# Optimization experiments

Measured on AMD Instinct MI355X. Metric: run time of the kernel, lower is better.

Reference implementation:

```python
import jax, jax.numpy as jnp
import numpy as np

BATCH, SEQ, H_IN, N_STATE, H_OUT = 16, 4096, 128, 256, 128
RMIN, RMAX, MAX_PHASE = 0.9, 1.0, 6.283


def setup_inputs() -> dict:
    key = jax.random.key(0)
    ks = jax.random.split(key, 9)
    u = jax.random.normal(ks[0], (BATCH, SEQ, H_IN), jnp.float32)
    # LRU exponential parameterization init (matches torch __init__)
    u1 = jax.random.uniform(ks[1], (N_STATE,), jnp.float32)
    u2 = jax.random.uniform(ks[2], (N_STATE,), jnp.float32)
    nu_log = jnp.log(-0.5 * jnp.log(u1 * (RMAX + RMIN) * (RMAX - RMIN) + RMIN ** 2))
    theta_log = jnp.log(MAX_PHASE * u2)
    lam_abs = jnp.exp(-jnp.exp(nu_log))
    gamma_log = jnp.log(jnp.sqrt(1.0 - lam_abs ** 2))
    s2in = np.sqrt(2.0 * H_IN).astype(np.float32)
    B_re = jax.random.normal(ks[3], (N_STATE, H_IN), jnp.float32) / s2in
    B_im = jax.random.normal(ks[4], (N_STATE, H_IN), jnp.float32) / s2in
    sst = np.sqrt(float(N_STATE)).astype(np.float32)
    C_re = jax.random.normal(ks[5], (H_OUT, N_STATE), jnp.float32) / sst
    C_im = jax.random.normal(ks[6], (H_OUT, N_STATE), jnp.float32) / sst
    D = jax.random.normal(ks[7], (H_OUT, H_IN), jnp.float32) / np.sqrt(float(H_IN)).astype(np.float32)
    return dict(u=u, nu_log=nu_log, theta_log=theta_log, gamma_log=gamma_log,
                B_re=B_re, B_im=B_im, C_re=C_re, C_im=C_im, D=D)


def _combine(a, b):
    # complex affine composition: (l, x) o (l', x') -> (l*l', l'*x + x')
    l1r, l1i, x1r, x1i = a
    l2r, l2i, x2r, x2i = b
    lr = l1r * l2r - l1i * l2i
    li = l1r * l2i + l1i * l2r
    xr = l2r * x1r - l2i * x1i + x2r
    xi = l2r * x1i + l2i * x1r + x2i
    return (lr, li, xr, xi)


def reference(u, nu_log, theta_log, gamma_log, B_re, B_im, C_re, C_im, D):
    lam_mod = jnp.exp(-jnp.exp(nu_log))          # |lambda|, [N]
    th = jnp.exp(theta_log)
    lam_re = lam_mod * jnp.cos(th)
    lam_im = lam_mod * jnp.sin(th)
    gammas = jnp.exp(gamma_log)                  # [N]
    # input projection Bu_t = gamma * (B @ u_t), complex -> real/imag parts
    Bu_re = jnp.einsum('blh,nh->bln', u, B_re) * gammas  # [B,L,N]
    Bu_im = jnp.einsum('blh,nh->bln', u, B_im) * gammas
    Bsz, L, N = Bu_re.shape
    lr = jnp.broadcast_to(lam_re, (Bsz, L, N))
    li = jnp.broadcast_to(lam_im, (Bsz, L, N))
    # parallel scan of x_t = lambda * x_{t-1} + Bu_t, x0 = 0
    _, _, xr, xi = jax.lax.associative_scan(_combine, (lr, li, Bu_re, Bu_im), axis=1)
    zero = jnp.zeros((Bsz, 1, N), u.dtype)
    pre_re = jnp.concatenate([zero, xr[:, :-1]], axis=1)  # states[:, :-1]
    pre_im = jnp.concatenate([zero, xi[:, :-1]], axis=1)
    # y_t = Re(C x_{t-1}) + D u_t
    y = (jnp.einsum('bln,on->blo', pre_re, C_re)
         - jnp.einsum('bln,on->blo', pre_im, C_im)
         + jnp.einsum('blh,oh->blo', u, D))
    return y
```

## Files before the change

kernel.cpp:

```cpp
#include <hip/hip_runtime.h>
#include <math.h>

#define BATCH 16
#define SEQ   4096
#define HIN   128
#define NST   256
#define HOUT  128
#define CL    32
#define NC    (SEQ/CL)
#define ROWS  (BATCH*SEQ)
#define KTOT  640
#define NPRE  512

typedef __attribute__((ext_vector_type(8))) short short8;
typedef __attribute__((ext_vector_type(4))) float f32x4;

__device__ inline unsigned short f2bf(float f) {
  union { float f; unsigned u; } v; v.f = f;
  unsigned r = v.u + 0x7FFFu + ((v.u >> 16) & 1u);
  return (unsigned short)(r >> 16);
}
__device__ inline float bf2f(unsigned short s) {
  union { unsigned u; float f; } v; v.u = ((unsigned)s) << 16;
  return v.f;
}
__device__ inline float bits2f(unsigned u) {
  union { unsigned u; float f; } v; v.u = u; return v.f;
}

__global__ __launch_bounds__(256) void k_prep(
    const float* __restrict__ nu_log, const float* __restrict__ theta_log,
    const float* __restrict__ gamma_log,
    const float* __restrict__ Bre, const float* __restrict__ Bim,
    const float* __restrict__ Cre, const float* __restrict__ Cim,
    const float* __restrict__ Dm,
    float* __restrict__ lamre, float* __restrict__ lamim,
    unsigned* __restrict__ lamPk,
    unsigned short* __restrict__ Wb, unsigned short* __restrict__ W) {
  int idx = blockIdx.x*256 + threadIdx.x;
  if (idx < NST) {
    float lm = expf(-expf(nu_log[idx]));
    float th = expf(theta_log[idx]);
    float lr = lm * cosf(th), li = lm * sinf(th);
    lamre[idx] = lr; lamim[idx] = li;
    float pr = 1.f, pi = 0.f;
    for (int j = 0; j < CL; ++j) {
      lamPk[j*NST + idx] = ((unsigned)f2bf(pi) << 16) | (unsigned)f2bf(pr);
      float nr = pr*lr - pi*li;
      float ni = pr*li + pi*lr;
      pr = nr; pi = ni;
    }
  }
  if (idx < 512*HIN) {
    int r = idx >> 7, h = idx & 127;
    int g = r >> 7;
    int w = r & 127;
    int n = g*64 + (w & 63);
    float gm = expf(gamma_log[n]);
    float v = (w < 64) ? Bre[n*HIN + h] : Bim[n*HIN + h];
    Wb[idx] = f2bf(gm * v);
  }
  if (idx < HOUT*KTOT) {
    int o = idx / KTOT, k = idx - o*KTOT;
    float v;
    if (k < NST)        v =  Cre[o*NST + k];
    else if (k < 2*NST) v = -Cim[o*NST + (k - NST)];
    else                v =  Dm[o*HIN + (k - 2*NST)];
    W[idx] = f2bf(v);
  }
}

union SharedBu {
  unsigned short B[128][136];
  unsigned short stgb[2][32][136];
};
__global__ __launch_bounds__(256) void k_bu(
    const float* __restrict__ u, const unsigned short* __restrict__ Wb,
    const float* __restrict__ lamre, const float* __restrict__ lamim,
    unsigned short* __restrict__ preL,
    float* __restrict__ S_re, float* __restrict__ S_im) {
  __shared__ unsigned short Asl[128][136];
  __shared__ SharedBu sh;
  int tid = threadIdx.x;
  int row0 = blockIdx.x * 128;
  int wid = tid >> 6, lane = tid & 63;
  int lm = lane & 15, lq = lane >> 4;
  int m0 = (wid >> 1) * 64, n0 = (wid & 1) * 64;
  int b = row0 >> 12;
  int cbase = (row0 & 4095) >> 5;
#pragma unroll
  for (int cc = 0; cc < 8; ++cc) {
    int ch = cc*256 + tid;
    int r = ch >> 4, h0 = (ch & 15) * 8;
    const float* src = u + (size_t)(row0 + r)*HIN + h0;
    float4 v0 = *(const float4*)src;
    float4 v1 = *(const float4*)(src + 4);
    unsigned short o[8];
    o[0]=f2bf(v0.x); o[1]=f2bf(v0.y); o[2]=f2bf(v0.z); o[3]=f2bf(v0.w);
    o[4]=f2bf(v1.x); o[5]=f2bf(v1.y); o[6]=f2bf(v1.z); o[7]=f2bf(v1.w);
    *(short8*)&Asl[r][h0] = *(const short8*)o;
  }
  for (int g = 0; g < 4; ++g) {
    __syncthreads();
#pragma unroll
    for (int cc = 0; cc < 8; ++cc) {
      int ch = cc*256 + tid;
      int r = ch >> 4, h0 = (ch & 15) * 8;
      *(short8*)&sh.B[r][h0] = *(const short8*)&Wb[(size_t)(g*128 + r)*HIN + h0];
    }
    __syncthreads();
    f32x4 acc[4][4];
#pragma unroll
    for (int i = 0; i < 4; ++i)
#pragma unroll
      for (int j = 0; j < 4; ++j) acc[i][j] = (f32x4)0.f;
#pragma unroll
    for (int ks = 0; ks < 4; ++ks) {
      int k0 = ks*32 + lq*8;
      short8 a[4], bb[4];
#pragma unroll
      for (int i = 0; i < 4; ++i) a[i] = *(const short8*)&Asl[m0 + i*16 + lm][k0];
#pragma unroll
      for (int j = 0; j < 4; ++j) bb[j] = *(const short8*)&sh.B[n0 + j*16 + lm][k0];
#pragma unroll
      for (int i = 0; i < 4; ++i)
#pragma unroll
        for (int j = 0; j < 4; ++j)
          acc[i][j] = __builtin_amdgcn_mfma_f32_16x16x32_bf16(a[i], bb[j], acc[i][j], 0, 0, 0);
    }
    for (int p = 0; p < 2; ++p) {
      __syncthreads();
#pragma unroll
      for (int ii = 0; ii < 2; ++ii) {
        int i = 2*p + ii;
#pragma unroll
        for (int j = 0; j < 4; ++j)
#pragma unroll
          for (int r = 0; r < 4; ++r) {
            int trow = ii*16 + lq*4 + r;
            sh.stgb[wid >> 1][trow][n0 + j*16 + lm] = f2bf(acc[i][j][r]);
          }
      }
      __syncthreads();
      if (tid < 128) {
        int buf = tid >> 6, nl = tid & 63;
        int ng = g*64 + nl;
        float lr = lamre[ng], li = lamim[ng];
        float rr[CL], ri[CL];
#pragma unroll
        for (int t = 0; t < CL; ++t) {
          rr[t] = bf2f(sh.stgb[buf][t][nl]);
          ri[t] = bf2f(sh.stgb[buf][t][64 + nl]);
        }
        float sr = 0.f, si = 0.f;
#pragma unroll
        for (int t = 0; t < CL; ++t) {
          sh.stgb[buf][t][nl]      = f2bf(sr);
          sh.stgb[buf][t][64 + nl] = f2bf(si);
          float nr = lr*sr - li*si + rr[t];
          float ni = lr*si + li*sr + ri[t];
          sr = nr; si = ni;
        }
        int c = cbase + buf*2 + p;
        int idx = (b*NC + c)*NST + ng;
        S_re[idx] = sr; S_im[idx] = si;
      }
      __syncthreads();
#pragma unroll
      for (int q = 0; q < 4; ++q) {
        int uidx = q*256 + tid;
        int buf = uidx >> 9;
        int rem = uidx & 511;
        int t   = rem >> 4;
        int seg = rem & 15;
        int im  = seg >> 3;
        int c0  = (seg & 7)*8 + im*64;
        int row = row0 + buf*64 + p*32 + t;
        int dcol = im*256 + g*64 + (seg & 7)*8;
        *(short8*)&preL[(size_t)row*NPRE + dcol] = *(const short8*)&sh.stgb[buf][t][c0];
      }
    }
  }
}

__global__ __launch_bounds__(64) void k_scan(
    const float* __restrict__ S_re, const float* __restrict__ S_im,
    const float* __restrict__ lamre, const float* __restrict__ lamim,
    unsigned* __restrict__ X0Pk) {
  int b = blockIdx.x >> 2;
  int n = (blockIdx.x & 3) * 64 + threadIdx.x;
  float ar = lamre[n], ai = lamim[n];
#pragma unroll
  for (int s = 0; s < 5; ++s) { float nr = ar*ar - ai*ai, ni = 2.f*ar*ai; ar = nr; ai = ni; }
  const float* Sr = S_re + (size_t)b*NC*NST + n;
  const float* Si = S_im + (size_t)b*NC*NST + n;
  unsigned* Xp = X0Pk + (size_t)b*NC*NST + n;
  float Are[16], Aim[16], Bre[16], Bim[16];
#pragma unroll
  for (int cc = 0; cc < 16; ++cc) { Are[cc] = Sr[cc*NST]; Aim[cc] = Si[cc*NST]; }
  float xr = 0.f, xi = 0.f;
#pragma unroll
  for (int seg = 0; seg < 8; ++seg) {
    if (seg < 7) {
      const float* pr = Sr + (size_t)(seg+1)*16*NST;
      const float* pi = Si + (size_t)(seg+1)*16*NST;
      if (seg & 1) {
#pragma unroll
        for (int cc = 0; cc < 16; ++cc) { Are[cc] = pr[cc*NST]; Aim[cc] = pi[cc*NST]; }
      } else {
#pragma unroll
        for (int cc = 0; cc < 16; ++cc) { Bre[cc] = pr[cc*NST]; Bim[cc] = pi[cc*NST]; }
      }
    }
#pragma unroll
    for (int cc = 0; cc < 16; ++cc) {
      Xp[(size_t)(seg*16 + cc)*NST] = ((unsigned)f2bf(xi) << 16) | (unsigned)f2bf(xr);
      float cr = (seg & 1) ? Bre[cc] : Are[cc];
      float ci = (seg & 1) ? Bim[cc] : Aim[cc];
      float nr = ar*xr - ai*xi + cr;
      float ni = ar*xi + ai*xr + ci;
      xr = nr; xi = ni;
    }
  }
}

__global__ __launch_bounds__(256) void k_out2(
    const unsigned short* __restrict__ preL, const float* __restrict__ u,
    const unsigned short* __restrict__ W,
    const unsigned* __restrict__ lamPk, const unsigned* __restrict__ X0Pk,
    float* __restrict__ y) {
  __shared__ unsigned short Asl[128][136];
  __shared__ unsigned short Bsl[128][136];
  int tid = threadIdx.x;
  int row0 = blockIdx.x * 128;
  int wid = tid >> 6, lane = tid & 63;
  int lm = lane & 15, lq = lane >> 4;
  int m0 = wid * 32;
  f32x4 acc[2][8];
#pragma unroll
  for (int i = 0; i < 2; ++i)
#pragma unroll
    for (int j = 0; j < 8; ++j) acc[i][j] = (f32x4)0.f;
  for (int s = 0; s < 5; ++s) {
    __syncthreads();
#pragma unroll
    for (int cc = 0; cc < 8; ++cc) {
      int ch = cc*256 + tid;
      int r = ch >> 4, h0 = (ch & 15) * 8;
      *(short8*)&Bsl[r][h0] = *(const short8*)&W[(size_t)r*KTOT + s*128 + h0];
    }
    if (s < 4) {
#pragma unroll
      for (int cc = 0; cc < 8; ++cc) {
        int ch = cc*256 + tid;
        int r = ch >> 4, h0 = (ch & 15) * 8;
        int grow = row0 + r;
        int j32 = r & 31;
        int cidx = grow >> 5;
        int n = ((s & 1) << 7) + h0;
        short8 loc = *(const short8*)&preL[(size_t)grow*NPRE + s*128 + h0];
        uint4 lp0 = *(const uint4*)&lamPk[j32*NST + n];
        uint4 lp1 = *(const uint4*)&lamPk[j32*NST + n + 4];
        uint4 xp0 = *(const uint4*)&X0Pk[(size_t)cidx*NST + n];
        uint4 xp1 = *(const uint4*)&X0Pk[(size_t)cidx*NST + n + 4];
        unsigned lps[8] = {lp0.x, lp0.y, lp0.z, lp0.w, lp1.x, lp1.y, lp1.z, lp1.w};
        unsigned xps[8] = {xp0.x, xp0.y, xp0.z, xp0.w, xp1.x, xp1.y, xp1.z, xp1.w};
        unsigned short o[8];
#pragma unroll
        for (int e = 0; e < 8; ++e) {
          float lr = bits2f(lps[e] << 16);
          float li = bits2f(lps[e] & 0xFFFF0000u);
          float xr = bits2f(xps[e] << 16);
          float xi = bits2f(xps[e] & 0xFFFF0000u);
          float lv = bf2f((unsigned short)loc[e]);
          float v = (s < 2) ? (lv + lr*xr - li*xi)
                            : (lv + lr*xi + li*xr);
          o[e] = f2bf(v);
        }
        *(short8*)&Asl[r][h0] = *(const short8*)o;
      }
    } else {
#pragma unroll
      for (int cc = 0; cc < 8; ++cc) {
        int ch = cc*256 + tid;
        int r = ch >> 4, h0 = (ch & 15) * 8;
        const float* src = u + (size_t)(row0 + r)*HIN + h0;
        float4 v0 = *(const float4*)src;
        float4 v1 = *(const float4*)(src + 4);
        unsigned short o[8];
        o[0]=f2bf(v0.x); o[1]=f2bf(v0.y); o[2]=f2bf(v0.z); o[3]=f2bf(v0.w);
        o[4]=f2bf(v1.x); o[5]=f2bf(v1.y); o[6]=f2bf(v1.z); o[7]=f2bf(v1.w);
        *(short8*)&Asl[r][h0] = *(const short8*)o;
      }
    }
    __syncthreads();
#pragma unroll
    for (int ks = 0; ks < 4; ++ks) {
      int k0 = ks*32 + lq*8;
      short8 a[2], bb[8];
#pragma unroll
      for (int i = 0; i < 2; ++i) a[i] = *(const short8*)&Asl[m0 + i*16 + lm][k0];
#pragma unroll
      for (int j = 0; j < 8; ++j) bb[j] = *(const short8*)&Bsl[j*16 + lm][k0];
#pragma unroll
      for (int i = 0; i < 2; ++i)
#pragma unroll
        for (int j = 0; j < 8; ++j)
          acc[i][j] = __builtin_amdgcn_mfma_f32_16x16x32_bf16(a[i], bb[j], acc[i][j], 0, 0, 0);
    }
  }
#pragma unroll
  for (int i = 0; i < 2; ++i)
#pragma unroll
    for (int j = 0; j < 8; ++j)
#pragma unroll
      for (int r = 0; r < 4; ++r)
        y[(size_t)(row0 + m0 + i*16 + lq*4 + r)*HOUT + j*16 + lm] = acc[i][j][r];
}

extern "C" void kernel_launch(void* const* d_in, const int* in_sizes, int n_in,
                              void* d_out, int out_size, void* d_ws, size_t ws_size,
                              hipStream_t stream) {
  const float* u         = (const float*)d_in[0];
  const float* nu_log    = (const float*)d_in[1];
  const float* theta_log = (const float*)d_in[2];
  const float* gamma_log = (const float*)d_in[3];
  const float* B_re      = (const float*)d_in[4];
  const float* B_im      = (const float*)d_in[5];
  const float* C_re      = (const float*)d_in[6];
  const float* C_im      = (const float*)d_in[7];
  const float* Dm        = (const float*)d_in[8];
  float* y = (float*)d_out;
  char* ws = (char*)d_ws;

  size_t off = 0;
  float* lamre = (float*)(ws + off);            off += 1024;
  float* lamim = (float*)(ws + off);            off += 1024;
  unsigned* lamPk = (unsigned*)(ws + off);      off += 32768;
  unsigned short* Wb = (unsigned short*)(ws + off); off += 131072;
  unsigned short* W  = (unsigned short*)(ws + off); off += 163840;
  unsigned short* preL = (unsigned short*)(ws + off); off += (size_t)ROWS*NPRE*2;
  float* S_re = (float*)(ws + off);             off += 2097152;
  float* S_im = (float*)(ws + off);             off += 2097152;
  unsigned* X0Pk = (unsigned*)(ws + off);       off += 2097152;

  k_prep<<<320, 256, 0, stream>>>(nu_log, theta_log, gamma_log, B_re, B_im,
                                  C_re, C_im, Dm, lamre, lamim, lamPk, Wb, W);
  k_bu<<<ROWS/128, 256, 0, stream>>>(u, Wb, lamre, lamim, preL, S_re, S_im);
  k_scan<<<64, 64, 0, stream>>>(S_re, S_im, lamre, lamim, X0Pk);
  k_out2<<<ROWS/128, 256, 0, stream>>>(preL, u, W, lamPk, X0Pk, y);
}
```

Before: 162.4 us.

## Recompute Bu projection in output kernel instead of materializing local states

The first pass now computes only the per-chunk end states and no longer writes the large bf16 local-state buffer (preL, 64 MB). The output kernel recomputes the B projection per 64-row tile, runs the intra-chunk recurrence seeded with the carried-in state, stages the states in shared memory, and feeds them straight into the C GEMM. Tile sizes are halved to 64 rows with launch-bounds occupancy hints. This removes a large global write and read at the cost of doing the input GEMM twice and running a serial scan inside the output kernel.

Result: slower. 174.9 us (+7.7%).

```diff
diff --git a/kernel.cpp b/kernel.cpp
--- a/kernel.cpp
+++ b/kernel.cpp
@@ -10,7 +10,6 @@
 #define NC    (SEQ/CL)
 #define ROWS  (BATCH*SEQ)
 #define KTOT  640
-#define NPRE  512
 
 typedef __attribute__((ext_vector_type(8))) short short8;
 typedef __attribute__((ext_vector_type(4))) float f32x4;
@@ -35,21 +34,13 @@
     const float* __restrict__ Cre, const float* __restrict__ Cim,
     const float* __restrict__ Dm,
     float* __restrict__ lamre, float* __restrict__ lamim,
-    unsigned* __restrict__ lamPk,
-    unsigned short* __restrict__ Wb, unsigned short* __restrict__ W) {
+    unsigned short* __restrict__ Wb, unsigned short* __restrict__ W2) {
   int idx = blockIdx.x*256 + threadIdx.x;
   if (idx < NST) {
     float lm = expf(-expf(nu_log[idx]));
     float th = expf(theta_log[idx]);
-    float lr = lm * cosf(th), li = lm * sinf(th);
-    lamre[idx] = lr; lamim[idx] = li;
-    float pr = 1.f, pi = 0.f;
-    for (int j = 0; j < CL; ++j) {
-      lamPk[j*NST + idx] = ((unsigned)f2bf(pi) << 16) | (unsigned)f2bf(pr);
-      float nr = pr*lr - pi*li;
-      float ni = pr*li + pi*lr;
-      pr = nr; pi = ni;
-    }
+    lamre[idx] = lm * cosf(th);
+    lamim[idx] = lm * sinf(th);
   }
   if (idx < 512*HIN) {
     int r = idx >> 7, h = idx & 127;
@@ -63,33 +54,36 @@
   if (idx < HOUT*KTOT) {
     int o = idx / KTOT, k = idx - o*KTOT;
     float v;
-    if (k < NST)        v =  Cre[o*NST + k];
-    else if (k < 2*NST) v = -Cim[o*NST + (k - NST)];
-    else                v =  Dm[o*HIN + (k - 2*NST)];
-    W[idx] = f2bf(v);
-  }
-}
-
-union SharedBu {
-  unsigned short B[128][136];
+    if (k < 512) {
+      int g = k >> 7, kk = k & 127;
+      int n = g*64 + (kk & 63);
+      v = (kk < 64) ? Cre[o*NST + n] : -Cim[o*NST + n];
+    } else {
+      v = Dm[o*HIN + (k - 512)];
+    }
+    W2[idx] = f2bf(v);
+  }
+}
+
+union SharedK1 {
+  unsigned short B[128][72];
   unsigned short stgb[2][32][136];
 };
-__global__ __launch_bounds__(256) void k_bu(
+__global__ __launch_bounds__(256, 4) void k_bu(
     const float* __restrict__ u, const unsigned short* __restrict__ Wb,
     const float* __restrict__ lamre, const float* __restrict__ lamim,
-    unsigned short* __restrict__ preL,
     float* __restrict__ S_re, float* __restrict__ S_im) {
-  __shared__ unsigned short Asl[128][136];
-  __shared__ SharedBu sh;
+  __shared__ unsigned short Asl[64][136];
+  __shared__ SharedK1 sh;
   int tid = threadIdx.x;
-  int row0 = blockIdx.x * 128;
+  int row0 = blockIdx.x * 64;
   int wid = tid >> 6, lane = tid & 63;
   int lm = lane & 15, lq = lane >> 4;
-  int m0 = (wid >> 1) * 64, n0 = (wid & 1) * 64;
+  int m0 = wid * 16;
   int b = row0 >> 12;
   int cbase = (row0 & 4095) >> 5;
 #pragma unroll
-  for (int cc = 0; cc < 8; ++cc) {
+  for (int cc = 0; cc < 4; ++cc) {
     int ch = cc*256 + tid;
     int r = ch >> 4, h0 = (ch & 15) * 8;
     const float* src = u + (size_t)(row0 + r)*HIN + h0;
@@ -101,84 +95,58 @@
     *(short8*)&Asl[r][h0] = *(const short8*)o;
   }
   for (int g = 0; g < 4; ++g) {
-    __syncthreads();
-#pragma unroll
-    for (int cc = 0; cc < 8; ++cc) {
-      int ch = cc*256 + tid;
-      int r = ch >> 4, h0 = (ch & 15) * 8;
-      *(short8*)&sh.B[r][h0] = *(const short8*)&Wb[(size_t)(g*128 + r)*HIN + h0];
-    }
-    __syncthreads();
-    f32x4 acc[4][4];
-#pragma unroll
-    for (int i = 0; i < 4; ++i)
-#pragma unroll
-      for (int j = 0; j < 4; ++j) acc[i][j] = (f32x4)0.f;
-#pragma unroll
-    for (int ks = 0; ks < 4; ++ks) {
-      int k0 = ks*32 + lq*8;
-      short8 a[4], bb[4];
-#pragma unroll
-      for (int i = 0; i < 4; ++i) a[i] = *(const short8*)&Asl[m0 + i*16 + lm][k0];
-#pragma unroll
-      for (int j = 0; j < 4; ++j) bb[j] = *(const short8*)&sh.B[n0 + j*16 + lm][k0];
-#pragma unroll
-      for (int i = 0; i < 4; ++i)
-#pragma unroll
-        for (int j = 0; j < 4; ++j)
-          acc[i][j] = __builtin_amdgcn_mfma_f32_16x16x32_bf16(a[i], bb[j], acc[i][j], 0, 0, 0);
-    }
-    for (int p = 0; p < 2; ++p) {
-      __syncthreads();
-#pragma unroll
-      for (int ii = 0; ii < 2; ++ii) {
-        int i = 2*p + ii;
-#pragma unroll
-        for (int j = 0; j < 4; ++j)
-#pragma unroll
-          for (int r = 0; r < 4; ++r) {
-            int trow = ii*16 + lq*4 + r;
-            sh.stgb[wid >> 1][trow][n0 + j*16 + lm] = f2bf(acc[i][j][r]);
-          }
-      }
-      __syncthreads();
-      if (tid < 128) {
-        int buf = tid >> 6, nl = tid & 63;
-        int ng = g*64 + nl;
-        float lr = lamre[ng], li = lamim[ng];
-        float rr[CL], ri[CL];
-#pragma unroll
-        for (int t = 0; t < CL; ++t) {
-          rr[t] = bf2f(sh.stgb[buf][t][nl]);
-          ri[t] = bf2f(sh.stgb[buf][t][64 + nl]);
+    f32x4 accB[8];
+#pragma unroll
+    for (int j = 0; j < 8; ++j) accB[j] = (f32x4)0.f;
+    for (int kh = 0; kh < 2; ++kh) {
+      __syncthreads();
+#pragma unroll
+      for (int cc = 0; cc < 4; ++cc) {
+        int ch = cc*256 + tid;
+        int r = ch >> 3, h0 = (ch & 7) * 8;
+        *(short8*)&sh.B[r][h0] = *(const short8*)&Wb[(size_t)(g*128 + r)*HIN + kh*64 + h0];
+      }
+      __syncthreads();
+#pragma unroll
+      for (int ks2 = 0; ks2 < 2; ++ks2) {
+        int k0 = (kh*2 + ks2)*32 + lq*8;
+        short8 a = *(const short8*)&Asl[m0 + lm][k0];
+#pragma unroll
+        for (int j = 0; j < 8; ++j) {
+          short8 bb = *(const short8*)&sh.B[j*16 + lm][k0 - kh*64];
+          accB[j] = __builtin_amdgcn_mfma_f32_16x16x32_bf16(a, bb, accB[j], 0, 0, 0);
         }
-        float sr = 0.f, si = 0.f;
-#pragma unroll
-        for (int t = 0; t < CL; ++t) {
-          sh.stgb[buf][t][nl]      = f2bf(sr);
-          sh.stgb[buf][t][64 + nl] = f2bf(si);
-          float nr = lr*sr - li*si + rr[t];
-          float ni = lr*si + li*sr + ri[t];
-          sr = nr; si = ni;
-        }
-        int c = cbase + buf*2 + p;
-        int idx = (b*NC + c)*NST + ng;
-        S_re[idx] = sr; S_im[idx] = si;
-      }
-      __syncthreads();
-#pragma unroll
-      for (int q = 0; q < 4; ++q) {
-        int uidx = q*256 + tid;
-        int buf = uidx >> 9;
-        int rem = uidx & 511;
-        int t   = rem >> 4;
-        int seg = rem & 15;
-        int im  = seg >> 3;
-        int c0  = (seg & 7)*8 + im*64;
-        int row = row0 + buf*64 + p*32 + t;
-        int dcol = im*256 + g*64 + (seg & 7)*8;
-        *(short8*)&preL[(size_t)row*NPRE + dcol] = *(const short8*)&sh.stgb[buf][t][c0];
-      }
+      }
+    }
+    __syncthreads();
+#pragma unroll
+    for (int j = 0; j < 8; ++j)
+#pragma unroll
+      for (int r = 0; r < 4; ++r) {
+        int row = m0 + lq*4 + r;
+        sh.stgb[row >> 5][row & 31][j*16 + lm] = f2bf(accB[j][r]);
+      }
+    __syncthreads();
+    if (tid < 128) {
+      int buf = tid >> 6, nl = tid & 63;
+      int ng = g*64 + nl;
+      float lr = lamre[ng], li = lamim[ng];
+      float rr[CL], ri[CL];
+#pragma unroll
+      for (int t = 0; t < CL; ++t) {
+        rr[t] = bf2f(sh.stgb[buf][t][nl]);
+        ri[t] = bf2f(sh.stgb[buf][t][64 + nl]);
+      }
+      float sr = 0.f, si = 0.f;
+#pragma unroll
+      for (int t = 0; t < CL; ++t) {
+        float nr = lr*sr - li*si + rr[t];
+        float ni = lr*si + li*sr + ri[t];
+        sr = nr; si = ni;
+      }
+      int c = cbase + buf;
+      int idx = (b*NC + c)*NST + ng;
+      S_re[idx] = sr; S_im[idx] = si;
     }
   }
 }
@@ -224,98 +192,137 @@
   }
 }
 
-__global__ __launch_bounds__(256) void k_out2(
-    const unsigned short* __restrict__ preL, const float* __restrict__ u,
-    const unsigned short* __restrict__ W,
-    const unsigned* __restrict__ lamPk, const unsigned* __restrict__ X0Pk,
+__global__ __launch_bounds__(256, 2) void k_out3(
+    const float* __restrict__ u, const unsigned short* __restrict__ Wb,
+    const unsigned short* __restrict__ W2,
+    const float* __restrict__ lamre, const float* __restrict__ lamim,
+    const unsigned* __restrict__ X0Pk,
     float* __restrict__ y) {
-  __shared__ unsigned short Asl[128][136];
-  __shared__ unsigned short Bsl[128][136];
+  __shared__ unsigned short Asl[64][136];
+  __shared__ unsigned short Bh[128][72];
+  __shared__ unsigned short stgb[2][32][136];
+  __shared__ unsigned short preS[64][136];
   int tid = threadIdx.x;
-  int row0 = blockIdx.x * 128;
+  int row0 = blockIdx.x * 64;
   int wid = tid >> 6, lane = tid & 63;
   int lm = lane & 15, lq = lane >> 4;
-  int m0 = wid * 32;
-  f32x4 acc[2][8];
-#pragma unroll
-  for (int i = 0; i < 2; ++i)
-#pragma unroll
-    for (int j = 0; j < 8; ++j) acc[i][j] = (f32x4)0.f;
-  for (int s = 0; s < 5; ++s) {
-    __syncthreads();
-#pragma unroll
-    for (int cc = 0; cc < 8; ++cc) {
+  int m0 = wid * 16;
+  int c0 = row0 >> 5;
+#pragma unroll
+  for (int cc = 0; cc < 4; ++cc) {
+    int ch = cc*256 + tid;
+    int r = ch >> 4, h0 = (ch & 15) * 8;
+    const float* src = u + (size_t)(row0 + r)*HIN + h0;
+    float4 v0 = *(const float4*)src;
+    float4 v1 = *(const float4*)(src + 4);
+    unsigned short o[8];
+    o[0]=f2bf(v0.x); o[1]=f2bf(v0.y); o[2]=f2bf(v0.z); o[3]=f2bf(v0.w);
+    o[4]=f2bf(v1.x); o[5]=f2bf(v1.y); o[6]=f2bf(v1.z); o[7]=f2bf(v1.w);
+    *(short8*)&Asl[r][h0] = *(const short8*)o;
+  }
+  f32x4 accY[8];
+#pragma unroll
+  for (int j = 0; j < 8; ++j) accY[j] = (f32x4)0.f;
+  for (int g = 0; g < 4; ++g) {
+    f32x4 accB[8];
+#pragma unroll
+    for (int j = 0; j < 8; ++j) accB[j] = (f32x4)0.f;
+    for (int kh = 0; kh < 2; ++kh) {
+      __syncthreads();
+#pragma unroll
+      for (int cc = 0; cc < 4; ++cc) {
+        int ch = cc*256 + tid;
+        int r = ch >> 3, h0 = (ch & 7) * 8;
+        *(short8*)&Bh[r][h0] = *(const short8*)&Wb[(size_t)(g*128 + r)*HIN + kh*64 + h0];
+      }
+      __syncthreads();
+#pragma unroll
+      for (int ks2 = 0; ks2 < 2; ++ks2) {
+        int k0 = (kh*2 + ks2)*32 + lq*8;
+        short8 a = *(const short8*)&Asl[m0 + lm][k0];
+#pragma unroll
+        for (int j = 0; j < 8; ++j) {
+          short8 bb = *(const short8*)&Bh[j*16 + lm][k0 - kh*64];
+          accB[j] = __builtin_amdgcn_mfma_f32_16x16x32_bf16(a, bb, accB[j], 0, 0, 0);
+        }
+      }
+    }
+#pragma unroll
+    for (int j = 0; j < 8; ++j)
+#pragma unroll
+      for (int r = 0; r < 4; ++r) {
+        int row = m0 + lq*4 + r;
+        stgb[row >> 5][row & 31][j*16 + lm] = f2bf(accB[j][r]);
+      }
+    __syncthreads();
+    if (tid < 128) {
+      int buf = tid >> 6, nl = tid & 63;
+      int ng = g*64 + nl;
+      float lr = lamre[ng], li = lamim[ng];
+      float rr[CL], ri[CL];
+#pragma unroll
+      for (int t = 0; t < CL; ++t) {
+        rr[t] = bf2f(stgb[buf][t][nl]);
+        ri[t] = bf2f(stgb[buf][t][64 + nl]);
+      }
+      unsigned xp = X0Pk[(size_t)(c0 + buf)*NST + ng];
+      float sr = bits2f(xp << 16), si = bits2f(xp & 0xFFFF0000u);
+#pragma unroll
+      for (int t = 0; t < CL; ++t) {
+        preS[buf*32 + t][nl]      = f2bf(sr);
+        preS[buf*32 + t][64 + nl] = f2bf(si);
+        float nr = lr*sr - li*si + rr[t];
+        float ni = lr*si + li*sr + ri[t];
+        sr = nr; si = ni;
+      }
+    }
+    __syncthreads();
+    for (int kh = 0; kh < 2; ++kh) {
+      if (kh) __syncthreads();
+#pragma unroll
+      for (int cc = 0; cc < 4; ++cc) {
+        int ch = cc*256 + tid;
+        int r = ch >> 3, h0 = (ch & 7) * 8;
+        *(short8*)&Bh[r][h0] = *(const short8*)&W2[(size_t)r*KTOT + g*128 + kh*64 + h0];
+      }
+      __syncthreads();
+#pragma unroll
+      for (int ks2 = 0; ks2 < 2; ++ks2) {
+        int k0 = (kh*2 + ks2)*32 + lq*8;
+        short8 a = *(const short8*)&preS[m0 + lm][k0];
+#pragma unroll
+        for (int j = 0; j < 8; ++j) {
+          short8 bb = *(const short8*)&Bh[j*16 + lm][k0 - kh*64];
+          accY[j] = __builtin_amdgcn_mfma_f32_16x16x32_bf16(a, bb, accY[j], 0, 0, 0);
+        }
+      }
+    }
+  }
+  for (int kh = 0; kh < 2; ++kh) {
+    __syncthreads();
+#pragma unroll
+    for (int cc = 0; cc < 4; ++cc) {
       int ch = cc*256 + tid;
-      int r = ch >> 4, h0 = (ch & 15) * 8;
-      *(short8*)&Bsl[r][h0] = *(const short8*)&W[(size_t)r*KTOT + s*128 + h0];
-    }
-    if (s < 4) {
-#pragma unroll
-      for (int cc = 0; cc < 8; ++cc) {
-        int ch = cc*256 + tid;
-        int r = ch >> 4, h0 = (ch & 15) * 8;
-        int grow = row0 + r;
-        int j32 = r & 31;
-        int cidx = grow >> 5;
-        int n = ((s & 1) << 7) + h0;
-        short8 loc = *(const short8*)&preL[(size_t)grow*NPRE + s*128 + h0];
-        uint4 lp0 = *(const uint4*)&lamPk[j32*NST + n];
-        uint4 lp1 = *(const uint4*)&lamPk[j32*NST + n + 4];
-        uint4 xp0 = *(const uint4*)&X0Pk[(size_t)cidx*NST + n];
-        uint4 xp1 = *(const uint4*)&X0Pk[(size_t)cidx*NST + n + 4];
-        unsigned lps[8] = {lp0.x, lp0.y, lp0.z, lp0.w, lp1.x, lp1.y, lp1.z, lp1.w};
-        unsigned xps[8] = {xp0.x, xp0.y, xp0.z, xp0.w, xp1.x, xp1.y, xp1.z, xp1.w};
-        unsigned short o[8];
-#pragma unroll
-        for (int e = 0; e < 8; ++e) {
-          float lr = bits2f(lps[e] << 16);
-          float li = bits2f(lps[e] & 0xFFFF0000u);
-          float xr = bits2f(xps[e] << 16);
-          float xi = bits2f(xps[e] & 0xFFFF0000u);
-          float lv = bf2f((unsigned short)loc[e]);
-          float v = (s < 2) ? (lv + lr*xr - li*xi)
-                            : (lv + lr*xi + li*xr);
-          o[e] = f2bf(v);
-        }
-        *(short8*)&Asl[r][h0] = *(const short8*)o;
-      }
-    } else {
-#pragma unroll
-      for (int cc = 0; cc < 8; ++cc) {
-        int ch = cc*256 + tid;
-        int r = ch >> 4, h0 = (ch & 15) * 8;
-        const float* src = u + (size_t)(row0 + r)*HIN + h0;
-        float4 v0 = *(const float4*)src;
-        float4 v1 = *(const float4*)(src + 4);
-        unsigned short o[8];
-        o[0]=f2bf(v0.x); o[1]=f2bf(v0.y); o[2]=f2bf(v0.z); o[3]=f2bf(v0.w);
-        o[4]=f2bf(v1.x); o[5]=f2bf(v1.y); o[6]=f2bf(v1.z); o[7]=f2bf(v1.w);
-        *(short8*)&Asl[r][h0] = *(const short8*)o;
-      }
-    }
-    __syncthreads();
-#pragma unroll
-    for (int ks = 0; ks < 4; ++ks) {
-      int k0 = ks*32 + lq*8;
-      short8 a[2], bb[8];
-#pragma unroll
-      for (int i = 0; i < 2; ++i) a[i] = *(const short8*)&Asl[m0 + i*16 + lm][k0];
-#pragma unroll
-      for (int j = 0; j < 8; ++j) bb[j] = *(const short8*)&Bsl[j*16 + lm][k0];
-#pragma unroll
-      for (int i = 0; i < 2; ++i)
-#pragma unroll
-        for (int j = 0; j < 8; ++j)
-          acc[i][j] = __builtin_amdgcn_mfma_f32_16x16x32_bf16(a[i], bb[j], acc[i][j], 0, 0, 0);
-    }
-  }
-#pragma unroll
-  for (int i = 0; i < 2; ++i)
-#pragma unroll
-    for (int j = 0; j < 8; ++j)
-#pragma unroll
-      for (int r = 0; r < 4; ++r)
-        y[(size_t)(row0 + m0 + i*16 + lq*4 + r)*HOUT + j*16 + lm] = acc[i][j][r];
+      int r = ch >> 3, h0 = (ch & 7) * 8;
+      *(short8*)&Bh[r][h0] = *(const short8*)&W2[(size_t)r*KTOT + 512 + kh*64 + h0];
+    }
+    __syncthreads();
+#pragma unroll
+    for (int ks2 = 0; ks2 < 2; ++ks2) {
+      int k0 = (kh*2 + ks2)*32 + lq*8;
+      short8 a = *(const short8*)&Asl[m0 + lm][k0];
+#pragma unroll
+      for (int j = 0; j < 8; ++j) {
+        short8 bb = *(const short8*)&Bh[j*16 + lm][k0 - kh*64];
+        accY[j] = __builtin_amdgcn_mfma_f32_16x16x32_bf16(a, bb, accY[j], 0, 0, 0);
+      }
+    }
+  }
+#pragma unroll
+  for (int j = 0; j < 8; ++j)
+#pragma unroll
+    for (int r = 0; r < 4; ++r)
+      y[(size_t)(row0 + m0 + lq*4 + r)*HOUT + j*16 + lm] = accY[j][r];
 }
 
 extern "C" void kernel_launch(void* const* d_in, const int* in_sizes, int n_in,
@@ -336,17 +343,15 @@
   size_t off = 0;
   float* lamre = (float*)(ws + off);            off += 1024;
   float* lamim = (float*)(ws + off);            off += 1024;
-  unsigned* lamPk = (unsigned*)(ws + off);      off += 32768;
   unsigned short* Wb = (unsigned short*)(ws + off); off += 131072;
-  unsigned short* W  = (unsigned short*)(ws + off); off += 163840;
-  unsigned short* preL = (unsigned short*)(ws + off); off += (size_t)ROWS*NPRE*2;
+  unsigned short* W2 = (unsigned short*)(ws + off); off += 163840;
   float* S_re = (float*)(ws + off);             off += 2097152;
   float* S_im = (float*)(ws + off);             off += 2097152;
   unsigned* X0Pk = (unsigned*)(ws + off);       off += 2097152;
 
   k_prep<<<320, 256, 0, stream>>>(nu_log, theta_log, gamma_log, B_re, B_im,
-                                  C_re, C_im, Dm, lamre, lamim, lamPk, Wb, W);
-  k_bu<<<ROWS/128, 256, 0, stream>>>(u, Wb, lamre, lamim, preL, S_re, S_im);
+                                  C_re, C_im, Dm, lamre, lamim, Wb, W2);
+  k_bu<<<ROWS/64, 256, 0, stream>>>(u, Wb, lamre, lamim, S_re, S_im);
   k_scan<<<64, 64, 0, stream>>>(S_re, S_im, lamre, lamim, X0Pk);
-  k_out2<<<ROWS/128, 256, 0, stream>>>(preL, u, W, lamPk, X0Pk, y);
-}
+  k_out3<<<ROWS/64, 256, 0, stream>>>(u, Wb, W2, lamre, lamim, X0Pk, y);
+}
```
